# Kernel tuning notes

Measured on AMD Instinct MI355X. Metric: run time of the kernel, lower is better.

## Reference

```python
import jax, jax.numpy as jnp
import numpy as np

BETA = 0.25  # commitment_beta


def setup_inputs() -> dict:
    key = jax.random.key(0)
    k1, k2 = jax.random.split(key)
    x = jax.random.normal(k1, (8, 256, 32, 32), dtype=jnp.float32)
    # nn.Embedding weight, uniform(-1/K, 1/K) in the original; use small randn-scaled init
    K, d = 4096, 256
    embed_w = jax.random.uniform(k2, (K, d), dtype=jnp.float32, minval=-1.0 / K, maxval=1.0 / K)
    return {"x": x, "embed_w": embed_w}


def reference(x, embed_w):
    B, C, H, W = x.shape
    N = H * W
    # b c h w -> b (h w) c
    xr = jnp.transpose(x, (0, 2, 3, 1)).reshape(B, N, C)
    flat = xr.reshape(B * N, C)
    dist = (-jnp.sum(flat * flat, axis=1, keepdims=True)
            - jnp.sum(embed_w * embed_w, axis=1)
            + 2.0 * jnp.einsum('nd,kd->nk', flat, embed_w))
    # temp=0.0 -> gumbel_sample degenerates to argmax
    embed_ind = jnp.argmax(dist, axis=-1).reshape(B, N)
    x_q = embed_w[embed_ind]  # [B, N, C] gather
    sg = jax.lax.stop_gradient
    loss = (BETA * jnp.mean((sg(x_q) - xr) ** 2)
            + jnp.mean((x_q - sg(xr)) ** 2))
    # straight-through estimator
    x_q = xr + sg(x_q - xr)
    # b (h w) c -> b c h w
    x_q = jnp.transpose(x_q.reshape(B, H, W, C), (0, 3, 1, 2))
    embed_ind = embed_ind.reshape(B, H, W)
    return (x_q, loss, embed_ind)
```

## Files before the change

kernel.cpp:

```cpp
#include <hip/hip_runtime.h>
#include <stdint.h>


typedef _Float16 f16;
typedef f16 half8 __attribute__((ext_vector_type(8)));
typedef float f32x4 __attribute__((ext_vector_type(4)));

__device__ __forceinline__ unsigned int sortable_f32(float v) {
    unsigned int u = __float_as_uint(v);
    return (u & 0x80000000u) ? ~u : (u | 0x80000000u);
}

__device__ __forceinline__ void gload_lds16(const void* g, void* l) {
    __builtin_amdgcn_global_load_lds(
        (const __attribute__((address_space(1))) unsigned int*)g,
        (__attribute__((address_space(3))) unsigned int*)l, 16, 0, 0);
}

__global__ void vq_pre(const float* __restrict__ x, const float* __restrict__ ew,
                       float* __restrict__ e2, float* __restrict__ negx2,
                       unsigned long long* __restrict__ cand,
                       float* __restrict__ loss_cell) {
    const int blk = blockIdx.x, tid = threadIdx.x;
    if (blk == 0 && tid == 0) *loss_cell = 0.0f;
    if (blk < 32) cand[blk * 256 + tid] = 0ull;
    if (blk < 16) {
        const int k = blk * 256 + tid;
        const float4* row = (const float4*)(ew + k * 256);
        float s = 0.0f;
#pragma unroll 8
        for (int i = 0; i < 64; ++i) {
            float4 v = row[i];
            s += v.x * v.x + v.y * v.y + v.z * v.z + v.w * v.w;
        }
        e2[k] = s;
    } else {
        const int r = (blk - 16) * 256 + tid;
        const int b = r >> 10, n = r & 1023;
        const float* px = x + b * 262144 + n;
        float s = 0.0f;
#pragma unroll 8
        for (int c = 0; c < 256; ++c) {
            float v = px[c << 10];
            s += v * v;
        }
        negx2[r] = -s;
    }
}

__global__ void split_e(const float* __restrict__ ew, f16* __restrict__ ehi, f16* __restrict__ elo) {
    const int t = blockIdx.x * 256 + threadIdx.x;
    const int k = t >> 5, g32 = t & 31;
    const float4 v0 = *(const float4*)(ew + k * 256 + g32 * 8);
    const float4 v1 = *(const float4*)(ew + k * 256 + g32 * 8 + 4);
    const float vf[8] = {v0.x, v0.y, v0.z, v0.w, v1.x, v1.y, v1.z, v1.w};
    half8 h1, h2;
#pragma unroll
    for (int j = 0; j < 8; ++j) {
        const float v = vf[j] * 4096.0f;
        const f16 a = (f16)v;
        const f16 b = (f16)(v - (float)a);
        h1[j] = a; h2[j] = b;
    }
    const int kt = k >> 7, kk = k & 127, ci = g32 >> 2, g = g32 & 3;
    const long off = ((long)((kt * 8 + ci) * 128 + kk)) * 32 + ((g ^ (kk & 3)) * 8);
    *(half8*)(ehi + off) = h1;
    *(half8*)(elo + off) = h2;
}

__global__ void split_x(const float* __restrict__ x, f16* __restrict__ xhi, f16* __restrict__ xlo) {
    __shared__ float xs[32][132];
    const int tid = threadIdx.x;
    const int ci = blockIdx.x, mt = blockIdx.y;
    const int b = mt >> 3, n0 = (mt & 7) * 128, c0 = ci * 32;
#pragma unroll
    for (int it = 0; it < 4; ++it) {
        const int idx = tid + it * 256;
        const int cc = idx >> 5, nn4 = idx & 31;
        float4 v = *(const float4*)(x + b * 262144 + (c0 + cc) * 1024 + n0 + nn4 * 4);
        *(float4*)&xs[cc][nn4 * 4] = v;
    }
    __syncthreads();
#pragma unroll
    for (int it = 0; it < 2; ++it) {
        const int idx = tid + it * 256;
        const int mm = idx & 127, g = idx >> 7;
        half8 h1, h2;
#pragma unroll
        for (int j = 0; j < 8; ++j) {
            const float v = xs[g * 8 + j][mm];
            const f16 a = (f16)v;
            const f16 bb = (f16)(v - (float)a);
            h1[j] = a; h2[j] = bb;
        }
        const long off = ((long)((mt * 8 + ci) * 128 + mm)) * 32 + ((g ^ (mm & 3)) * 8);
        *(half8*)(xhi + off) = h1;
        *(half8*)(xlo + off) = h2;
    }
}

__launch_bounds__(256, 2)
__global__ void vq_gemm(const f16* __restrict__ xhi, const f16* __restrict__ xlo,
                        const f16* __restrict__ ehi, const f16* __restrict__ elo,
                        const float* __restrict__ e2, const float* __restrict__ negx2,
                        unsigned long long* __restrict__ cand) {
    __shared__ __align__(16) f16 lds[16384];
    const int tid = threadIdx.x;
    const int kt = blockIdx.x, mt = blockIdx.y;
    const int lane = tid & 63, wave = tid >> 6;
    const int wm = wave >> 1, wk = wave & 1;
    const int col = lane & 15, quad = lane >> 4;

    f32x4 acc[4][4] = {};

    const f16* gx[2] = { xhi + (size_t)(mt * 8) * 4096, xlo + (size_t)(mt * 8) * 4096 };
    const f16* ge[2] = { ehi + (size_t)(kt * 8) * 4096, elo + (size_t)(kt * 8) * 4096 };

    int aoff[4], boff[4];
#pragma unroll
    for (int i = 0; i < 4; ++i) {
        const int m = wm * 64 + i * 16 + col;
        aoff[i] = m * 32 + ((quad ^ (m & 3)) * 8);
        const int k = wk * 64 + i * 16 + col;
        boff[i] = k * 32 + ((quad ^ (k & 3)) * 8);
    }

    for (int ci = 0; ci < 8; ++ci) {
        __syncthreads();
        const int go = ci * 4096 + tid * 8;
        char* lb = (char*)lds + (tid >> 6) * 1024;
#pragma unroll
        for (int p = 0; p < 2; ++p) {
            gload_lds16(gx[p] + go,        lb + p * 8192);
            gload_lds16(gx[p] + go + 2048, lb + p * 8192 + 4096);
            gload_lds16(ge[p] + go,        lb + 16384 + p * 8192);
            gload_lds16(ge[p] + go + 2048, lb + 16384 + p * 8192 + 4096);
        }
        __syncthreads();

        half8 ahi[4], alo[4], bhi[4], blo[4];
#pragma unroll
        for (int i = 0; i < 4; ++i) {
            ahi[i] = *(const half8*)&lds[aoff[i]];
            alo[i] = *(const half8*)&lds[4096 + aoff[i]];
            bhi[i] = *(const half8*)&lds[8192 + boff[i]];
            blo[i] = *(const half8*)&lds[12288 + boff[i]];
        }
#pragma unroll
        for (int i = 0; i < 4; ++i)
#pragma unroll
            for (int j = 0; j < 4; ++j) {
                acc[i][j] = __builtin_amdgcn_mfma_f32_16x16x32_f16(ahi[i], bhi[j], acc[i][j], 0, 0, 0);
                acc[i][j] = __builtin_amdgcn_mfma_f32_16x16x32_f16(ahi[i], blo[j], acc[i][j], 0, 0, 0);
                acc[i][j] = __builtin_amdgcn_mfma_f32_16x16x32_f16(alo[i], bhi[j], acc[i][j], 0, 0, 0);
            }
    }

    const int m0 = mt * 128 + wm * 64, k0 = kt * 128 + wk * 64;
    unsigned long long best[4][4];
#pragma unroll
    for (int i = 0; i < 4; ++i)
#pragma unroll
        for (int r = 0; r < 4; ++r) {
            const float A = negx2[m0 + i * 16 + quad * 4 + r];
            unsigned long long bk = 0ull;
#pragma unroll
            for (int j = 0; j < 4; ++j) {
                const int k = k0 + j * 16 + col;
                const float t1 = A - e2[k];
                const float dist = t1 + acc[i][j][r] * 0x1p-11f;
                const unsigned long long key =
                    ((unsigned long long)sortable_f32(dist) << 32)
                    | (unsigned long long)(unsigned int)(4095 - k);
                bk = key > bk ? key : bk;
            }
            best[i][r] = bk;
        }
#pragma unroll
    for (int i = 0; i < 4; ++i)
#pragma unroll
        for (int r = 0; r < 4; ++r) {
#pragma unroll
            for (int mask = 1; mask <= 8; mask <<= 1) {
                const unsigned long long o = __shfl_xor(best[i][r], mask, 64);
                if (o > best[i][r]) best[i][r] = o;
            }
            if (col == i * 4 + r)
                atomicMax(&cand[m0 + i * 16 + quad * 4 + r], best[i][r]);
        }
}

__global__ void vq_out(const float* __restrict__ x, const float* __restrict__ ew,
                       const unsigned long long* __restrict__ cand,
                       float* __restrict__ out) {
    __shared__ int sidx[64];
    __shared__ float wsum[4];
    const int tid = threadIdx.x;
    const int r0 = blockIdx.x * 64;
    const int b = r0 >> 10, n0 = r0 & 1023;

    if (tid < 64) {
        const int r = r0 + tid;
        const unsigned long long bk = cand[r];
        const int idx = 4095 - (int)(unsigned int)(bk & 0xFFFFFFFFull);
        sidx[tid] = idx;
        out[2097153 + r] = (float)idx;
    }
    __syncthreads();

    const int nn = tid & 63, cq = tid >> 6;
    const int myidx = sidx[nn];
    float lsum = 0.0f;
#pragma unroll 4
    for (int cb = 0; cb < 256; cb += 4) {
        const int c = cb + cq;
        const float ve = ew[myidx * 256 + c];
        const long off = (long)b * 262144 + (c << 10) + n0 + nn;
        const float vx = x[off];
        out[off] = ve;
        const float d = ve - vx;
        lsum += d * d;
    }
#pragma unroll
    for (int off = 32; off > 0; off >>= 1)
        lsum += __shfl_down(lsum, off, 64);
    const int lane = tid & 63, w = tid >> 6;
    if (lane == 0) wsum[w] = lsum;
    __syncthreads();
    if (tid == 0) {
        const float s = wsum[0] + wsum[1] + wsum[2] + wsum[3];
        atomicAdd(&out[2097152], 1.25f * (s / 2097152.0f));
    }
}

extern "C" void kernel_launch(void* const* d_in, const int* in_sizes, int n_in,
                              void* d_out, int out_size, void* d_ws, size_t ws_size,
                              hipStream_t stream) {
    const float* x  = (const float*)d_in[0];
    const float* ew = (const float*)d_in[1];
    float* out = (float*)d_out;

    float* e2 = (float*)d_ws;
    float* negx2 = e2 + 4096;
    unsigned long long* cand = (unsigned long long*)((char*)d_ws + 49152);
    f16* ehi = (f16*)((char*)d_ws + 114688);
    f16* elo = (f16*)((char*)d_ws + 114688 + 2097152);
    f16* xhi = (f16*)out;
    f16* xlo = (f16*)(out + 1048576);

    vq_pre<<<48, 256, 0, stream>>>(x, ew, e2, negx2, cand, out + 2097152);
    split_e<<<512, 256, 0, stream>>>(ew, ehi, elo);
    split_x<<<dim3(8, 64), 256, 0, stream>>>(x, xhi, xlo);
    vq_gemm<<<dim3(32, 64), 256, 0, stream>>>(xhi, xlo, ehi, elo, e2, negx2, cand);
    vq_out<<<128, 256, 0, stream>>>(x, ew, cand, out);
}
```

Measured before the change: 165.7 us.

## Use 32x32 MFMA with 256-row tiles, fuse prep kernels, split output across channels

The GEMM now uses 32x32x16 MFMA instructions on a larger 256x128 block tile with a 48KB LDS buffer, halving the number of M blocks and improving operand reuse per LDS load. The prep kernels are merged: codebook split and norms go in one launch, and the x-norm is computed inside the x split via atomicAdd instead of a separate strided pass. The output kernel is split four ways across channels for more parallelism. The larger LDS footprint and accumulator count may lower occupancy.

```diff
diff --git a/kernel.cpp b/kernel.cpp
--- a/kernel.cpp
+++ b/kernel.cpp
@@ -4,7 +4,7 @@
 
 typedef _Float16 f16;
 typedef f16 half8 __attribute__((ext_vector_type(8)));
-typedef float f32x4 __attribute__((ext_vector_type(4)));
+typedef float f32x16 __attribute__((ext_vector_type(16)));
 
 __device__ __forceinline__ unsigned int sortable_f32(float v) {
     unsigned int u = __float_as_uint(v);
@@ -17,15 +17,31 @@
         (__attribute__((address_space(3))) unsigned int*)l, 16, 0, 0);
 }
 
-__global__ void vq_pre(const float* __restrict__ x, const float* __restrict__ ew,
-                       float* __restrict__ e2, float* __restrict__ negx2,
-                       unsigned long long* __restrict__ cand,
-                       float* __restrict__ loss_cell) {
+__global__ void vq_prep_e(const float* __restrict__ ew, f16* __restrict__ ehi,
+                          f16* __restrict__ elo, float* __restrict__ e2,
+                          unsigned long long* __restrict__ cand,
+                          float* __restrict__ negx2, float* __restrict__ loss_cell) {
     const int blk = blockIdx.x, tid = threadIdx.x;
-    if (blk == 0 && tid == 0) *loss_cell = 0.0f;
-    if (blk < 32) cand[blk * 256 + tid] = 0ull;
-    if (blk < 16) {
-        const int k = blk * 256 + tid;
+    if (blk < 512) {
+        const int t = blk * 256 + tid;
+        const int k = t >> 5, g32 = t & 31;
+        const float4 v0 = *(const float4*)(ew + k * 256 + g32 * 8);
+        const float4 v1 = *(const float4*)(ew + k * 256 + g32 * 8 + 4);
+        const float vf[8] = {v0.x, v0.y, v0.z, v0.w, v1.x, v1.y, v1.z, v1.w};
+        half8 h1, h2;
+#pragma unroll
+        for (int j = 0; j < 8; ++j) {
+            const float v = vf[j] * 4096.0f;
+            const f16 a = (f16)v;
+            const f16 b = (f16)(v - (float)a);
+            h1[j] = a; h2[j] = b;
+        }
+        const int kt = k >> 7, kk = k & 127, ci = g32 >> 2, g = g32 & 3;
+        const long off = ((long)((kt * 8 + ci) * 128 + kk)) * 32 + ((g ^ (kk & 3)) * 8);
+        *(half8*)(ehi + off) = h1;
+        *(half8*)(elo + off) = h2;
+    } else if (blk < 528) {
+        const int k = (blk - 512) * 256 + tid;
         const float4* row = (const float4*)(ew + k * 256);
         float s = 0.0f;
 #pragma unroll 8
@@ -35,40 +51,15 @@
         }
         e2[k] = s;
     } else {
-        const int r = (blk - 16) * 256 + tid;
-        const int b = r >> 10, n = r & 1023;
-        const float* px = x + b * 262144 + n;
-        float s = 0.0f;
-#pragma unroll 8
-        for (int c = 0; c < 256; ++c) {
-            float v = px[c << 10];
-            s += v * v;
-        }
-        negx2[r] = -s;
-    }
-}
-
-__global__ void split_e(const float* __restrict__ ew, f16* __restrict__ ehi, f16* __restrict__ elo) {
-    const int t = blockIdx.x * 256 + threadIdx.x;
-    const int k = t >> 5, g32 = t & 31;
-    const float4 v0 = *(const float4*)(ew + k * 256 + g32 * 8);
-    const float4 v1 = *(const float4*)(ew + k * 256 + g32 * 8 + 4);
-    const float vf[8] = {v0.x, v0.y, v0.z, v0.w, v1.x, v1.y, v1.z, v1.w};
-    half8 h1, h2;
-#pragma unroll
-    for (int j = 0; j < 8; ++j) {
-        const float v = vf[j] * 4096.0f;
-        const f16 a = (f16)v;
-        const f16 b = (f16)(v - (float)a);
-        h1[j] = a; h2[j] = b;
-    }
-    const int kt = k >> 7, kk = k & 127, ci = g32 >> 2, g = g32 & 3;
-    const long off = ((long)((kt * 8 + ci) * 128 + kk)) * 32 + ((g ^ (kk & 3)) * 8);
-    *(half8*)(ehi + off) = h1;
-    *(half8*)(elo + off) = h2;
-}
-
-__global__ void split_x(const float* __restrict__ x, f16* __restrict__ xhi, f16* __restrict__ xlo) {
+        const int z = (blk - 528) * 256 + tid;
+        cand[z] = 0ull;
+        negx2[z] = 0.0f;
+        if (z == 0) *loss_cell = 0.0f;
+    }
+}
+
+__global__ void vq_prep_x(const float* __restrict__ x, f16* __restrict__ xhi,
+                          f16* __restrict__ xlo, float* __restrict__ negx2) {
     __shared__ float xs[32][132];
     const int tid = threadIdx.x;
     const int ci = blockIdx.x, mt = blockIdx.y;
@@ -81,22 +72,29 @@
         *(float4*)&xs[cc][nn4 * 4] = v;
     }
     __syncthreads();
+    const int mt256 = mt >> 1;
+    float sq = 0.0f;
+    int mm_g = 0;
 #pragma unroll
     for (int it = 0; it < 2; ++it) {
         const int idx = tid + it * 256;
         const int mm = idx & 127, g = idx >> 7;
+        mm_g = mm;
         half8 h1, h2;
 #pragma unroll
         for (int j = 0; j < 8; ++j) {
             const float v = xs[g * 8 + j][mm];
+            sq += v * v;
             const f16 a = (f16)v;
             const f16 bb = (f16)(v - (float)a);
             h1[j] = a; h2[j] = bb;
         }
-        const long off = ((long)((mt * 8 + ci) * 128 + mm)) * 32 + ((g ^ (mm & 3)) * 8);
+        const int mm256 = (mt & 1) * 128 + mm;
+        const long off = ((long)((mt256 * 8 + ci) * 256 + mm256)) * 32 + ((g ^ (mm256 & 3)) * 8);
         *(half8*)(xhi + off) = h1;
         *(half8*)(xlo + off) = h2;
     }
+    atomicAdd(&negx2[mt * 128 + mm_g], -sq);
 }
 
 __launch_bounds__(256, 2)
@@ -104,90 +102,102 @@
                         const f16* __restrict__ ehi, const f16* __restrict__ elo,
                         const float* __restrict__ e2, const float* __restrict__ negx2,
                         unsigned long long* __restrict__ cand) {
-    __shared__ __align__(16) f16 lds[16384];
+    __shared__ __align__(16) f16 lds[24576];
     const int tid = threadIdx.x;
     const int kt = blockIdx.x, mt = blockIdx.y;
     const int lane = tid & 63, wave = tid >> 6;
     const int wm = wave >> 1, wk = wave & 1;
-    const int col = lane & 15, quad = lane >> 4;
-
-    f32x4 acc[4][4] = {};
-
-    const f16* gx[2] = { xhi + (size_t)(mt * 8) * 4096, xlo + (size_t)(mt * 8) * 4096 };
-    const f16* ge[2] = { ehi + (size_t)(kt * 8) * 4096, elo + (size_t)(kt * 8) * 4096 };
-
-    int aoff[4], boff[4];
+    const int l31 = lane & 31, hl = lane >> 5;
+
+    const f16* gxh = xhi + (size_t)(mt * 8) * 8192;
+    const f16* gxl = xlo + (size_t)(mt * 8) * 8192;
+    const f16* geh = ehi + (size_t)(kt * 8) * 4096;
+    const f16* gel = elo + (size_t)(kt * 8) * 4096;
+
+    f32x16 acc[4][2] = {};
+
+    int aoff[4][2], boff[2][2];
 #pragma unroll
     for (int i = 0; i < 4; ++i) {
-        const int m = wm * 64 + i * 16 + col;
-        aoff[i] = m * 32 + ((quad ^ (m & 3)) * 8);
-        const int k = wk * 64 + i * 16 + col;
-        boff[i] = k * 32 + ((quad ^ (k & 3)) * 8);
+        const int mr = wm * 128 + i * 32 + l31;
+#pragma unroll
+        for (int ks = 0; ks < 2; ++ks)
+            aoff[i][ks] = mr * 32 + (((ks * 2 + hl) ^ (mr & 3)) * 8);
+    }
+#pragma unroll
+    for (int j = 0; j < 2; ++j) {
+        const int kr = wk * 64 + j * 32 + l31;
+#pragma unroll
+        for (int ks = 0; ks < 2; ++ks)
+            boff[j][ks] = 16384 + kr * 32 + (((ks * 2 + hl) ^ (kr & 3)) * 8);
     }
 
     for (int ci = 0; ci < 8; ++ci) {
         __syncthreads();
-        const int go = ci * 4096 + tid * 8;
-        char* lb = (char*)lds + (tid >> 6) * 1024;
-#pragma unroll
-        for (int p = 0; p < 2; ++p) {
-            gload_lds16(gx[p] + go,        lb + p * 8192);
-            gload_lds16(gx[p] + go + 2048, lb + p * 8192 + 4096);
-            gload_lds16(ge[p] + go,        lb + 16384 + p * 8192);
-            gload_lds16(ge[p] + go + 2048, lb + 16384 + p * 8192 + 4096);
-        }
+        const int t8 = tid * 8;
+        char* wb = (char*)lds + (tid >> 6) * 1024;
+#pragma unroll
+        for (int p = 0; p < 4; ++p) gload_lds16(gxh + ci * 8192 + p * 2048 + t8, wb + p * 4096);
+#pragma unroll
+        for (int p = 0; p < 4; ++p) gload_lds16(gxl + ci * 8192 + p * 2048 + t8, wb + 16384 + p * 4096);
+#pragma unroll
+        for (int p = 0; p < 2; ++p) gload_lds16(geh + ci * 4096 + p * 2048 + t8, wb + 32768 + p * 4096);
+#pragma unroll
+        for (int p = 0; p < 2; ++p) gload_lds16(gel + ci * 4096 + p * 2048 + t8, wb + 40960 + p * 4096);
         __syncthreads();
 
-        half8 ahi[4], alo[4], bhi[4], blo[4];
-#pragma unroll
-        for (int i = 0; i < 4; ++i) {
-            ahi[i] = *(const half8*)&lds[aoff[i]];
-            alo[i] = *(const half8*)&lds[4096 + aoff[i]];
-            bhi[i] = *(const half8*)&lds[8192 + boff[i]];
-            blo[i] = *(const half8*)&lds[12288 + boff[i]];
-        }
-#pragma unroll
-        for (int i = 0; i < 4; ++i)
-#pragma unroll
-            for (int j = 0; j < 4; ++j) {
-                acc[i][j] = __builtin_amdgcn_mfma_f32_16x16x32_f16(ahi[i], bhi[j], acc[i][j], 0, 0, 0);
-                acc[i][j] = __builtin_amdgcn_mfma_f32_16x16x32_f16(ahi[i], blo[j], acc[i][j], 0, 0, 0);
-                acc[i][j] = __builtin_amdgcn_mfma_f32_16x16x32_f16(alo[i], bhi[j], acc[i][j], 0, 0, 0);
-            }
-    }
-
-    const int m0 = mt * 128 + wm * 64, k0 = kt * 128 + wk * 64;
-    unsigned long long best[4][4];
-#pragma unroll
-    for (int i = 0; i < 4; ++i)
-#pragma unroll
-        for (int r = 0; r < 4; ++r) {
-            const float A = negx2[m0 + i * 16 + quad * 4 + r];
+#pragma unroll
+        for (int ks = 0; ks < 2; ++ks) {
+            half8 ah[4], al[4], bh[2], bl[2];
+#pragma unroll
+            for (int i = 0; i < 4; ++i) {
+                ah[i] = *(const half8*)&lds[aoff[i][ks]];
+                al[i] = *(const half8*)&lds[8192 + aoff[i][ks]];
+            }
+#pragma unroll
+            for (int j = 0; j < 2; ++j) {
+                bh[j] = *(const half8*)&lds[boff[j][ks]];
+                bl[j] = *(const half8*)&lds[4096 + boff[j][ks]];
+            }
+#pragma unroll
+            for (int i = 0; i < 4; ++i)
+#pragma unroll
+                for (int j = 0; j < 2; ++j) {
+                    acc[i][j] = __builtin_amdgcn_mfma_f32_32x32x16_f16(ah[i], bh[j], acc[i][j], 0, 0, 0);
+                    acc[i][j] = __builtin_amdgcn_mfma_f32_32x32x16_f16(ah[i], bl[j], acc[i][j], 0, 0, 0);
+                    acc[i][j] = __builtin_amdgcn_mfma_f32_32x32x16_f16(al[i], bh[j], acc[i][j], 0, 0, 0);
+                }
+        }
+    }
+
+    const int m0g = mt * 256 + wm * 128;
+    const int k0g = kt * 128 + wk * 64;
+#pragma unroll
+    for (int i = 0; i < 4; ++i) {
+#pragma unroll
+        for (int r = 0; r < 16; ++r) {
+            const int row = (r & 3) + 8 * (r >> 2) + 4 * hl;
+            const int mg = m0g + i * 32 + row;
+            const float A = negx2[mg];
             unsigned long long bk = 0ull;
 #pragma unroll
-            for (int j = 0; j < 4; ++j) {
-                const int k = k0 + j * 16 + col;
-                const float t1 = A - e2[k];
+            for (int j = 0; j < 2; ++j) {
+                const int kg = k0g + j * 32 + l31;
+                const float t1 = A - e2[kg];
                 const float dist = t1 + acc[i][j][r] * 0x1p-11f;
                 const unsigned long long key =
                     ((unsigned long long)sortable_f32(dist) << 32)
-                    | (unsigned long long)(unsigned int)(4095 - k);
-                bk = key > bk ? key : bk;
-            }
-            best[i][r] = bk;
-        }
-#pragma unroll
-    for (int i = 0; i < 4; ++i)
-#pragma unroll
-        for (int r = 0; r < 4; ++r) {
-#pragma unroll
-            for (int mask = 1; mask <= 8; mask <<= 1) {
-                const unsigned long long o = __shfl_xor(best[i][r], mask, 64);
-                if (o > best[i][r]) best[i][r] = o;
-            }
-            if (col == i * 4 + r)
-                atomicMax(&cand[m0 + i * 16 + quad * 4 + r], best[i][r]);
-        }
+                    | (unsigned long long)(unsigned int)(4095 - kg);
+                if (key > bk) bk = key;
+            }
+#pragma unroll
+            for (int mask = 1; mask <= 16; mask <<= 1) {
+                const unsigned long long o = __shfl_xor(bk, mask, 64);
+                if (o > bk) bk = o;
+            }
+            if (l31 == r) atomicMax(&cand[mg], bk);
+        }
+    }
 }
 
 __global__ void vq_out(const float* __restrict__ x, const float* __restrict__ ew,
@@ -197,6 +207,7 @@
     __shared__ float wsum[4];
     const int tid = threadIdx.x;
     const int r0 = blockIdx.x * 64;
+    const int cq0 = blockIdx.y * 64;
     const int b = r0 >> 10, n0 = r0 & 1023;
 
     if (tid < 64) {
@@ -204,7 +215,7 @@
         const unsigned long long bk = cand[r];
         const int idx = 4095 - (int)(unsigned int)(bk & 0xFFFFFFFFull);
         sidx[tid] = idx;
-        out[2097153 + r] = (float)idx;
+        if (blockIdx.y == 0) out[2097153 + r] = (float)idx;
     }
     __syncthreads();
 
@@ -212,8 +223,8 @@
     const int myidx = sidx[nn];
     float lsum = 0.0f;
 #pragma unroll 4
-    for (int cb = 0; cb < 256; cb += 4) {
-        const int c = cb + cq;
+    for (int cb = 0; cb < 16; ++cb) {
+        const int c = cq0 + cb * 4 + cq;
         const float ve = ew[myidx * 256 + c];
         const long off = (long)b * 262144 + (c << 10) + n0 + nn;
         const float vx = x[off];
@@ -248,9 +259,8 @@
     f16* xhi = (f16*)out;
     f16* xlo = (f16*)(out + 1048576);
 
-    vq_pre<<<48, 256, 0, stream>>>(x, ew, e2, negx2, cand, out + 2097152);
-    split_e<<<512, 256, 0, stream>>>(ew, ehi, elo);
-    split_x<<<dim3(8, 64), 256, 0, stream>>>(x, xhi, xlo);
-    vq_gemm<<<dim3(32, 64), 256, 0, stream>>>(xhi, xlo, ehi, elo, e2, negx2, cand);
-    vq_out<<<128, 256, 0, stream>>>(x, ew, cand, out);
-}
+    vq_prep_e<<<560, 256, 0, stream>>>(ew, ehi, elo, e2, cand, negx2, out + 2097152);
+    vq_prep_x<<<dim3(8, 64), 256, 0, stream>>>(x, xhi, xlo, negx2);
+    vq_gemm<<<dim3(32, 32), 256, 0, stream>>>(xhi, xlo, ehi, elo, e2, negx2, cand);
+    vq_out<<<dim3(128, 4), 256, 0, stream>>>(x, ew, cand, out);
+}
```

After: 212.3 us. +28.1%, slower.
